# Kernel optimization log

Measured on AMD Instinct MI355X. Metric: run time of the kernel, lower is better.

Reference implementation:

```python
import jax, jax.numpy as jnp
import numpy as np

P = 7          # window size
HEADS = 8
DIM_HEAD = 32
INNER = HEADS * DIM_HEAD  # 256
DIM_IN = 256
DIM_OUT = 256
SCALE = DIM_HEAD ** -0.5


def _rel_index(p):
    i = np.array([[x, y] for x in range(p) for y in range(p)])  # (p*p, 2)
    d = i[None, :, :] - i[:, None, :]                            # (p*p, p*p, 2)
    return jnp.asarray(d + p - 1, dtype=jnp.int32)


def setup_inputs() -> dict:
    key = jax.random.key(0)
    ks = jax.random.split(key, 6)
    x = jax.random.normal(ks[0], (16, DIM_IN, 112, 112), dtype=jnp.float32)
    Wq = jax.random.normal(ks[1], (INNER, DIM_IN), dtype=jnp.float32) * 0.02
    Wkv = jax.random.normal(ks[2], (2 * INNER, DIM_IN), dtype=jnp.float32) * 0.02
    Wo = jax.random.normal(ks[3], (DIM_OUT, INNER), dtype=jnp.float32) * 0.02
    bo = jax.random.normal(ks[4], (DIM_OUT,), dtype=jnp.float32) * 0.02
    pos_embedding = jax.random.normal(ks[5], (2 * P - 1, 2 * P - 1), dtype=jnp.float32) * 0.02
    rel_index = _rel_index(P)
    return {"x": x, "Wq": Wq, "Wkv": Wkv, "Wo": Wo, "bo": bo,
            "pos_embedding": pos_embedding, "rel_index": rel_index}


def _local_attention(x, Wq, Wkv, Wo, bo, pos_embedding, rel_index):
    b, c, h, w = x.shape
    n1, n2 = h // P, w // P
    n = P * P
    # relative position bias (p^2, p^2)
    bias = pos_embedding[rel_index[:, :, 0], rel_index[:, :, 1]]
    # window partition: (b, c, n1, P, n2, P) -> (b*n1*n2, c, P*P)
    xw = x.reshape(b, c, n1, P, n2, P).transpose(0, 2, 4, 1, 3, 5)
    xw = xw.reshape(b * n1 * n2, c, n)
    # 1x1 conv projections as channel GEMMs
    q = jnp.einsum('oc,bcn->bon', Wq, xw)       # (B', INNER, n)
    kv = jnp.einsum('oc,bcn->bon', Wkv, xw)     # (B', 2*INNER, n)
    k, v = kv[:, :INNER], kv[:, INNER:]

    def to_heads(t):  # (B', H*d, n) -> (B', H, n, d)
        Bp = t.shape[0]
        return t.reshape(Bp, HEADS, DIM_HEAD, n).transpose(0, 1, 3, 2)

    q, k, v = to_heads(q), to_heads(k), to_heads(v)
    dots = jnp.einsum('bhid,bhjd->bhij', q, k) * SCALE + bias
    attn = jax.nn.softmax(dots, axis=-1)
    out = jnp.einsum('bhij,bhjd->bhid', attn, v)          # (B', H, n, d)
    out = out.transpose(0, 1, 3, 2).reshape(-1, INNER, n)  # (B', H*d, n)
    out = jnp.einsum('oc,bcn->bon', Wo, out) + bo[None, :, None]
    # window merge back to (b, c_out, h, w)
    out = out.reshape(b, n1, n2, DIM_OUT, P, P).transpose(0, 3, 1, 4, 2, 5)
    out = out.reshape(b, DIM_OUT, h, w)
    return out, attn


def reference(x, Wq, Wkv, Wo, bo, pos_embedding, rel_index):
    return _local_attention(x, Wq, Wkv, Wo, bo, pos_embedding, rel_index)
```

## Files before the change

### kernel.cpp

```cpp
#include <hip/hip_runtime.h>
#include <hip/hip_bf16.h>

typedef __bf16 bf16x8 __attribute__((ext_vector_type(8)));
typedef __bf16 bf16x4 __attribute__((ext_vector_type(4)));
typedef float  f32x4  __attribute__((ext_vector_type(4)));
typedef float  f32x16 __attribute__((ext_vector_type(16)));
typedef float  f32x4a __attribute__((ext_vector_type(4))) __attribute__((aligned(4)));
typedef float  f32x2a __attribute__((ext_vector_type(2))) __attribute__((aligned(4)));

#define NPOS 49
#define NHEADS 8
#define SCALE_F 0.17677669529663687f

#define SLICE_B   16896
#define QK_ROW_B  264
#define VS_OFF    8192
#define VS_ROW_B  136
#define XWT_PITCH 264
#define AOT_PITCH 264
#define BIAS_OFF  67584
#define BO_OFF    77188
#define LDS_BYTES 78212

static __device__ __forceinline__ f32x16 zero16() {
  f32x16 z;
#pragma unroll
  for (int i = 0; i < 16; ++i) z[i] = 0.f;
  return z;
}

__global__ void prep_kernel(const float* __restrict__ Wq, const float* __restrict__ Wkv,
                            const float* __restrict__ Wo, const float* __restrict__ pos,
                            const int* __restrict__ rel, __bf16* __restrict__ wqkv,
                            __bf16* __restrict__ wo, float* __restrict__ bias,
                            __bf16* __restrict__ wqkvP, __bf16* __restrict__ woP) {
  const int idx = blockIdx.x * 256 + threadIdx.x;
  const int row = idx >> 8, col = idx & 255;
  const float wv = (row < 256) ? Wq[idx] : Wkv[idx - 65536];
  wqkv[idx] = (__bf16)wv;
  {
    const int s = row >> 5, l31 = row & 31;
    const int ks = col >> 4, g2 = (col >> 3) & 1, e = col & 7;
    wqkvP[((size_t)((s * 16 + ks) * 64 + g2 * 32 + l31)) * 8 + e] = (__bf16)wv;
  }
  if (idx < 65536) {
    const float w = Wo[idx];
    wo[idx] = (__bf16)w;
    const int t = row >> 4, c16 = row & 15;
    const int kk = col >> 5, g4 = (col >> 3) & 3, e = col & 7;
    woP[((size_t)((t * 8 + kk) * 64 + g4 * 16 + c16)) * 8 + e] = (__bf16)w;
  }
  if (idx < 49 * 49) bias[idx] = pos[rel[idx * 2] * 13 + rel[idx * 2 + 1]];
}

template <int MODE>
__global__ __launch_bounds__(256, 2) void attn_kernel(
    const float* __restrict__ x, const __bf16* __restrict__ wqkvP,
    const __bf16* __restrict__ wo, const float* __restrict__ bias_g,
    const float* __restrict__ bo_g, float* __restrict__ outg,
    float* __restrict__ attng, __bf16* __restrict__ aoT_g) {
  extern __shared__ char smem[];
  __bf16* xwT = (__bf16*)smem;
  __bf16* aoT = (__bf16*)smem;
  float* bias_s = (float*)(smem + BIAS_OFF);
  float* bo_s   = (float*)(smem + BO_OFF);

  const int tid = threadIdx.x;
  const int bid = blockIdx.x;
  const int work = (bid & 7) * 512 + (bid >> 3);
  const int b  = work >> 8;
  const int i1 = (work >> 4) & 15;
  const int i2 = work & 15;
  const int r0 = i1 * 7, c0 = i2 * 7;
  const int wave = tid >> 6, lane = tid & 63;
  const int l31 = lane & 31, g2 = lane >> 5;
  const int c16 = lane & 15, g4 = lane >> 4;
  char* slice = smem + wave * SLICE_B;

  {
    bf16x8 z8;
#pragma unroll
    for (int j = 0; j < 8; ++j) z8[j] = (__bf16)0.f;
    for (int i = tid; i < 480; i += 256) {
      const int row = 49 + (i >> 5);
      const int col = (i & 31) * 8;
      *(bf16x8*)(xwT + row * XWT_PITCH + col) = z8;
    }
    f32x4a b4[7]; f32x2a b2[7]; float b1[7];
    int chv[7], rowv[7];
    const float* xb = x + (size_t)b * 256 * 12544;
#pragma unroll
    for (int k = 0; k < 7; ++k) {
      const int p = k * 256 + tid;
      const int ch = p / 7;
      const int row = p - ch * 7;
      chv[k] = ch; rowv[k] = row;
      const float* xr = xb + (size_t)ch * 12544 + (size_t)(r0 + row) * 112 + c0;
      b4[k] = *(const f32x4a*)xr;
      b2[k] = *(const f32x2a*)(xr + 4);
      b1[k] = xr[6];
    }
#pragma unroll
    for (int k = 0; k < 7; ++k) {
      __bf16* dst = xwT + (rowv[k] * 7) * XWT_PITCH + chv[k];
      dst[0 * XWT_PITCH] = (__bf16)b4[k][0];
      dst[1 * XWT_PITCH] = (__bf16)b4[k][1];
      dst[2 * XWT_PITCH] = (__bf16)b4[k][2];
      dst[3 * XWT_PITCH] = (__bf16)b4[k][3];
      dst[4 * XWT_PITCH] = (__bf16)b2[k][0];
      dst[5 * XWT_PITCH] = (__bf16)b2[k][1];
      dst[6 * XWT_PITCH] = (__bf16)b1[k];
    }
    const float4* bg4 = (const float4*)bias_g;
    for (int i = tid; i < 600; i += 256) ((float4*)bias_s)[i] = bg4[i];
    if (tid == 0) bias_s[2400] = bias_g[2400];
    if constexpr (MODE == 0) bo_s[tid] = bo_g[tid];
  }
  __syncthreads();

  bf16x8 Bf0[16], Bf1[16];
  {
    const __bf16* Bp = xwT + l31 * XWT_PITCH + g2 * 8;
#pragma unroll
    for (int ks = 0; ks < 16; ++ks) {
      Bf0[ks] = *(const bf16x8*)(Bp + ks * 16);
      Bf1[ks] = *(const bf16x8*)(Bp + 32 * XWT_PITCH + ks * 16);
    }
  }
  __syncthreads();

  char* vsb = slice + VS_OFF;
  {
    const __bf16* A0p = wqkvP + (size_t)(16 + 2 * wave) * 8192 + lane * 8;
    const __bf16* A1p = A0p + 8192;
    f32x16 a00 = zero16(), a01 = zero16(), a10 = zero16(), a11 = zero16();
    __builtin_amdgcn_s_setprio(1);
#pragma unroll
    for (int ks = 0; ks < 16; ++ks) {
      bf16x8 A0 = *(const bf16x8*)(A0p + ks * 512);
      bf16x8 A1 = *(const bf16x8*)(A1p + ks * 512);
      a00 = __builtin_amdgcn_mfma_f32_32x32x16_bf16(A0, Bf0[ks], a00, 0, 0, 0);
      a01 = __builtin_amdgcn_mfma_f32_32x32x16_bf16(A0, Bf1[ks], a01, 0, 0, 0);
      a10 = __builtin_amdgcn_mfma_f32_32x32x16_bf16(A1, Bf0[ks], a10, 0, 0, 0);
      a11 = __builtin_amdgcn_mfma_f32_32x32x16_bf16(A1, Bf1[ks], a11, 0, 0, 0);
    }
    __builtin_amdgcn_s_setprio(0);
#pragma unroll
    for (int rg = 0; rg < 16; ++rg) {
      const int dd = (rg & 3) + 8 * (rg >> 2) + 4 * g2;
      *(__bf16*)(vsb + dd * VS_ROW_B + l31 * 2)              = (__bf16)a00[rg];
      *(__bf16*)(vsb + dd * VS_ROW_B + 64 + l31 * 2)         = (__bf16)a01[rg];
      *(__bf16*)(vsb + (32 + dd) * VS_ROW_B + l31 * 2)       = (__bf16)a10[rg];
      *(__bf16*)(vsb + (32 + dd) * VS_ROW_B + 64 + l31 * 2)  = (__bf16)a11[rg];
    }
  }
  bf16x8 vf[2][2][2];
#pragma unroll
  for (int hh = 0; hh < 2; ++hh)
#pragma unroll
    for (int nt = 0; nt < 2; ++nt)
#pragma unroll
      for (int ks = 0; ks < 2; ++ks)
        vf[hh][nt][ks] = *(const bf16x8*)(vsb + (hh * 32 + nt * 16 + c16) * VS_ROW_B + ks * 64 + g4 * 16);
  asm volatile("s_waitcnt lgkmcnt(0)" ::: "memory");
  __builtin_amdgcn_sched_barrier(0x20);

#pragma unroll
  for (int qk = 0; qk < 2; ++qk) {
    const int koff = qk * 64;
    const __bf16* A0p = wqkvP + (size_t)(2 * wave + qk * 8) * 8192 + lane * 8;
    const __bf16* A1p = A0p + 8192;
    f32x16 a00 = zero16(), a01 = zero16(), a10 = zero16(), a11 = zero16();
    __builtin_amdgcn_s_setprio(1);
#pragma unroll
    for (int ks = 0; ks < 16; ++ks) {
      bf16x8 A0 = *(const bf16x8*)(A0p + ks * 512);
      bf16x8 A1 = *(const bf16x8*)(A1p + ks * 512);
      a00 = __builtin_amdgcn_mfma_f32_32x32x16_bf16(A0, Bf0[ks], a00, 0, 0, 0);
      a01 = __builtin_amdgcn_mfma_f32_32x32x16_bf16(A0, Bf1[ks], a01, 0, 0, 0);
      a10 = __builtin_amdgcn_mfma_f32_32x32x16_bf16(A1, Bf0[ks], a10, 0, 0, 0);
      a11 = __builtin_amdgcn_mfma_f32_32x32x16_bf16(A1, Bf1[ks], a11, 0, 0, 0);
    }
    __builtin_amdgcn_s_setprio(0);
#define STORE_QK(ACC, P_, NT)                                                  \
    {                                                                          \
      const int n_ = (NT) * 32 + l31;                                          \
      _Pragma("unroll") for (int rb = 0; rb < 4; ++rb) {                       \
        const int ddb = koff + (P_) * 32 + rb * 8 + g2 * 4;                    \
        bf16x4 v4;                                                             \
        v4[0] = (__bf16)ACC[rb * 4 + 0]; v4[1] = (__bf16)ACC[rb * 4 + 1];      \
        v4[2] = (__bf16)ACC[rb * 4 + 2]; v4[3] = (__bf16)ACC[rb * 4 + 3];      \
        *(bf16x4*)(slice + n_ * QK_ROW_B + ddb * 2) = v4;                      \
      }                                                                        \
    }
    STORE_QK(a00, 0, 0)
    STORE_QK(a01, 0, 1)
    STORE_QK(a10, 1, 0)
    STORE_QK(a11, 1, 1)
  }
  bf16x8 qf[2][4], kf[2][4];
#pragma unroll
  for (int hh = 0; hh < 2; ++hh)
#pragma unroll
    for (int t = 0; t < 4; ++t) {
      qf[hh][t] = *(const bf16x8*)(slice + (t * 16 + c16) * QK_ROW_B + hh * 64 + g4 * 16);
      kf[hh][t] = *(const bf16x8*)(slice + (t * 16 + c16) * QK_ROW_B + 128 + hh * 64 + g4 * 16);
    }
  asm volatile("s_waitcnt lgkmcnt(0)" ::: "memory");
  __builtin_amdgcn_sched_barrier(0x20);

  f32x4 pacc[2][4][2];
  char* Pb0 = slice;
  char* Pb1 = slice + 8192;
  {
    const f32x4 z4 = {0.f, 0.f, 0.f, 0.f};
    f32x4 dacc[2][4][4];
    __builtin_amdgcn_s_setprio(1);
#pragma unroll
    for (int hh = 0; hh < 2; ++hh)
#pragma unroll
      for (int mt = 0; mt < 4; ++mt)
#pragma unroll
        for (int nt = 0; nt < 4; ++nt)
          dacc[hh][mt][nt] = __builtin_amdgcn_mfma_f32_16x16x32_bf16(qf[hh][mt], kf[hh][nt], z4, 0, 0, 0);
    __builtin_amdgcn_s_setprio(0);

    const int h0 = wave * 2;
#pragma unroll
    for (int mt = 0; mt < 4; ++mt) {
#pragma unroll
      for (int r = 0; r < 4; ++r) {
        const int i = mt * 16 + g4 * 4 + r;
        float p0[4], p1[4], s0 = 0.f, s1 = 0.f;
#pragma unroll
        for (int nt = 0; nt < 4; ++nt) {
          const int j = nt * 16 + c16;
          float v0 = dacc[0][mt][nt][r] * SCALE_F;
          float v1 = dacc[1][mt][nt][r] * SCALE_F;
          if (j < NPOS) {
            if (i < NPOS) { const float bb = bias_s[i * 49 + j]; v0 += bb; v1 += bb; }
          } else {
            v0 = -1e30f; v1 = -1e30f;
          }
          p0[nt] = __expf(v0); s0 += p0[nt];
          p1[nt] = __expf(v1); s1 += p1[nt];
        }
        s0 += __shfl_xor(s0, 1); s1 += __shfl_xor(s1, 1);
        s0 += __shfl_xor(s0, 2); s1 += __shfl_xor(s1, 2);
        s0 += __shfl_xor(s0, 4); s1 += __shfl_xor(s1, 4);
        s0 += __shfl_xor(s0, 8); s1 += __shfl_xor(s1, 8);
        const float inv0 = 1.f / s0, inv1 = 1.f / s1;
        if (i < NPOS) {
          float* ap0 = attng + ((size_t)(work * NHEADS + h0) * 49 + i) * 49;
          float* ap1 = ap0 + 49 * 49;
#pragma unroll
          for (int nt = 0; nt < 4; ++nt) {
            const int j = nt * 16 + c16;
            if (j < NPOS) { ap0[j] = p0[nt] * inv0; ap1[j] = p1[nt] * inv1; }
          }
        }
#pragma unroll
        for (int nt = 0; nt < 4; ++nt) {
          const int j = nt * 16 + c16;
          *(__bf16*)(Pb0 + i * 128 + 16 * ((j >> 3) ^ (i & 7)) + 2 * (j & 7)) = (__bf16)(p0[nt] * inv0);
          *(__bf16*)(Pb1 + i * 128 + 16 * ((j >> 3) ^ (i & 7)) + 2 * (j & 7)) = (__bf16)(p1[nt] * inv1);
        }
      }
    }

    __builtin_amdgcn_s_setprio(1);
#pragma unroll
    for (int hh = 0; hh < 2; ++hh) {
      char* Pb = hh ? Pb1 : Pb0;
#pragma unroll
      for (int mt = 0; mt < 4; ++mt) {
        const int i = mt * 16 + c16;
        bf16x8 pa0 = *(const bf16x8*)(Pb + i * 128 + 16 * ((0 + g4) ^ (i & 7)));
        bf16x8 pa1 = *(const bf16x8*)(Pb + i * 128 + 16 * ((4 + g4) ^ (i & 7)));
#pragma unroll
        for (int nt = 0; nt < 2; ++nt) {
          f32x4 acc = {0.f, 0.f, 0.f, 0.f};
          acc = __builtin_amdgcn_mfma_f32_16x16x32_bf16(pa0, vf[hh][nt][0], acc, 0, 0, 0);
          acc = __builtin_amdgcn_mfma_f32_16x16x32_bf16(pa1, vf[hh][nt][1], acc, 0, 0, 0);
          pacc[hh][mt][nt] = acc;
        }
      }
    }
    __builtin_amdgcn_s_setprio(0);
  }

  if constexpr (MODE == 1) {
    __bf16* ag = aoT_g + (size_t)work * 12544;
#pragma unroll
    for (int hh = 0; hh < 2; ++hh) {
      const int h = wave * 2 + hh;
#pragma unroll
      for (int mt = 0; mt < 4; ++mt)
#pragma unroll
        for (int e = 0; e < 4; ++e) {
          const int pos = mt * 16 + g4 * 4 + e;
          if (pos < NPOS) {
            ag[pos * 256 + h * 32 + c16]      = (__bf16)pacc[hh][mt][0][e];
            ag[pos * 256 + h * 32 + 16 + c16] = (__bf16)pacc[hh][mt][1][e];
          }
        }
    }
  } else {
    __syncthreads();
#pragma unroll
    for (int hh = 0; hh < 2; ++hh) {
      const int h = wave * 2 + hh;
#pragma unroll
      for (int mt = 0; mt < 4; ++mt)
#pragma unroll
        for (int nt = 0; nt < 2; ++nt)
#pragma unroll
          for (int e = 0; e < 4; ++e) {
            const int i = mt * 16 + g4 * 4 + e;
            const int cc = h * 32 + nt * 16 + c16;
            aoT[i * AOT_PITCH + cc] = (__bf16)pacc[hh][mt][nt][e];
          }
    }
    __syncthreads();
    {
      bf16x8 Cf0[16], Cf1[16];
      const __bf16* Bp = aoT + l31 * AOT_PITCH + g2 * 8;
#pragma unroll
      for (int ks = 0; ks < 16; ++ks) {
        Cf0[ks] = *(const bf16x8*)(Bp + ks * 16);
        Cf1[ks] = *(const bf16x8*)(Bp + 32 * AOT_PITCH + ks * 16);
      }
      const __bf16* Ap0 = wo + (size_t)(wave * 64 + l31) * 256 + g2 * 8;
      const __bf16* Ap1 = Ap0 + 32 * 256;
      f32x16 a00 = zero16(), a01 = zero16(), a10 = zero16(), a11 = zero16();
      __builtin_amdgcn_s_setprio(1);
#pragma unroll
      for (int ks = 0; ks < 16; ++ks) {
        bf16x8 A0 = *(const bf16x8*)(Ap0 + ks * 16);
        bf16x8 A1 = *(const bf16x8*)(Ap1 + ks * 16);
        a00 = __builtin_amdgcn_mfma_f32_32x32x16_bf16(A0, Cf0[ks], a00, 0, 0, 0);
        a01 = __builtin_amdgcn_mfma_f32_32x32x16_bf16(A0, Cf1[ks], a01, 0, 0, 0);
        a10 = __builtin_amdgcn_mfma_f32_32x32x16_bf16(A1, Cf0[ks], a10, 0, 0, 0);
        a11 = __builtin_amdgcn_mfma_f32_32x32x16_bf16(A1, Cf1[ks], a11, 0, 0, 0);
      }
      __builtin_amdgcn_s_setprio(0);
      float* og = outg + (size_t)b * 256 * 12544;
#define STORE_OUT(ACC, MT, NT)                                                    \
      {                                                                           \
        const int n_ = (NT) * 32 + l31;                                           \
        if (n_ < NPOS) {                                                          \
          const int pr_ = n_ / 7, pc_ = n_ - pr_ * 7;                             \
          float* orow = og + (size_t)(r0 + pr_) * 112 + (c0 + pc_);               \
          _Pragma("unroll") for (int rg = 0; rg < 16; ++rg) {                     \
            const int o2 = wave * 64 + (MT) * 32 + (rg & 3) + 8 * (rg >> 2) + 4 * g2; \
            orow[(size_t)o2 * 12544] = ACC[rg] + bo_s[o2];                        \
          }                                                                       \
        }                                                                         \
      }
      STORE_OUT(a00, 0, 0)
      STORE_OUT(a01, 0, 1)
      STORE_OUT(a10, 1, 0)
      STORE_OUT(a11, 1, 1)
    }
  }
}

__global__ __launch_bounds__(256, 2) void oproj_kernel(
    const __bf16* __restrict__ aoT_g, const __bf16* __restrict__ woP,
    const float* __restrict__ bo_g, float* __restrict__ outg) {
  __shared__ __bf16 aoB[112 * 264];
  __shared__ float bo_s[256];
  const int tid = threadIdx.x;
  const int bid = blockIdx.x;
  const int work = (bid & 7) * 224 + (bid >> 3);
  const int pr = work % 7;
  const int g  = work / 7;
  const int i1 = g & 15, b = g >> 4;
  const int wave = tid >> 6, lane = tid & 63;
  const int c16 = lane & 15, g4 = lane >> 4;

  {
    const int rr = tid >> 5, coff = (tid & 31) * 8;
#pragma unroll
    for (int it = 0; it < 14; ++it) {
      const int gr = it * 8 + rr;
      const int i2 = gr / 7, pc = gr - i2 * 7;
      const size_t src = ((size_t)((b * 256 + i1 * 16 + i2) * 49 + pr * 7 + pc)) * 256 + coff;
      *(bf16x8*)(aoB + gr * 264 + coff) = *(const bf16x8*)(aoT_g + src);
    }
    bo_s[tid] = bo_g[tid];
  }
  __syncthreads();

  const int oc0 = wave * 64;
  const __bf16* Ap = woP + ((size_t)wave * 4 * 8) * 512 + lane * 8;
  f32x4 acc[4][7];
#pragma unroll
  for (int mt = 0; mt < 4; ++mt)
#pragma unroll
    for (int nt = 0; nt < 7; ++nt) acc[mt][nt] = f32x4{0.f, 0.f, 0.f, 0.f};
#pragma unroll
  for (int kk = 0; kk < 8; ++kk) {
    bf16x8 Af[4], Bf[7];
#pragma unroll
    for (int mt = 0; mt < 4; ++mt)
      Af[mt] = *(const bf16x8*)(Ap + (size_t)(mt * 8 + kk) * 512);
#pragma unroll
    for (int nt = 0; nt < 7; ++nt)
      Bf[nt] = *(const bf16x8*)(aoB + (nt * 16 + c16) * 264 + kk * 32 + g4 * 8);
    __builtin_amdgcn_s_setprio(1);
#pragma unroll
    for (int mt = 0; mt < 4; ++mt)
#pragma unroll
      for (int nt = 0; nt < 7; ++nt)
        acc[mt][nt] = __builtin_amdgcn_mfma_f32_16x16x32_bf16(Af[mt], Bf[nt], acc[mt][nt], 0, 0, 0);
    __builtin_amdgcn_s_setprio(0);
  }
  float* orow = outg + (size_t)b * 256 * 12544 + (size_t)(i1 * 7 + pr) * 112;
#pragma unroll
  for (int mt = 0; mt < 4; ++mt)
#pragma unroll
    for (int e = 0; e < 4; ++e) {
      const int oc = oc0 + mt * 16 + g4 * 4 + e;
      const float bb = bo_s[oc];
#pragma unroll
      for (int nt = 0; nt < 7; ++nt)
        orow[(size_t)oc * 12544 + nt * 16 + c16] = acc[mt][nt][e] + bb;
    }
}

extern "C" void kernel_launch(void* const* d_in, const int* in_sizes, int n_in,
                              void* d_out, int out_size, void* d_ws, size_t ws_size,
                              hipStream_t stream) {
  const float* x   = (const float*)d_in[0];
  const float* Wq  = (const float*)d_in[1];
  const float* Wkv = (const float*)d_in[2];
  const float* Wo  = (const float*)d_in[3];
  const float* bo  = (const float*)d_in[4];
  const float* pos = (const float*)d_in[5];
  const int*   rel = (const int*)d_in[6];

  float* outg  = (float*)d_out;
  float* attng = outg + (size_t)16 * 256 * 112 * 112;

  __bf16* wqkv  = (__bf16*)d_ws;
  __bf16* wo    = (__bf16*)((char*)d_ws + 393216);
  float*  bias  = (float*)((char*)d_ws + 393216 + 131072);
  __bf16* wqkvP = (__bf16*)((char*)d_ws + 393216 + 131072 + 9728);
  __bf16* woP   = (__bf16*)((char*)d_ws + 393216 + 131072 + 9728 + 393216);
  size_t base = 393216 + 131072 + 9728 + 393216 + 131072;
  base = (base + 255) & ~(size_t)255;
  const size_t ao_bytes = (size_t)4096 * 12544 * 2;
  __bf16* aoT_g = (__bf16*)((char*)d_ws + base);
  (void)wqkv;

  hipFuncSetAttribute((const void*)attn_kernel<0>,
                      hipFuncAttributeMaxDynamicSharedMemorySize, LDS_BYTES);
  hipFuncSetAttribute((const void*)attn_kernel<1>,
                      hipFuncAttributeMaxDynamicSharedMemorySize, LDS_BYTES);

  prep_kernel<<<dim3(768), dim3(256), 0, stream>>>(Wq, Wkv, Wo, pos, rel, wqkv, wo, bias,
                                                   wqkvP, woP);
  if (ws_size >= base + ao_bytes) {
    attn_kernel<1><<<dim3(4096), dim3(256), LDS_BYTES, stream>>>(
        x, wqkvP, wo, bias, bo, outg, attng, aoT_g);
    oproj_kernel<<<dim3(1792), dim3(256), 0, stream>>>(aoT_g, woP, bo, outg);
  } else {
    attn_kernel<0><<<dim3(4096), dim3(256), LDS_BYTES, stream>>>(
        x, wqkvP, wo, bias, bo, outg, attng, nullptr);
  }
}
```

Before: 426.0 us.

## Shrink per-wave LDS slices and read bias from global to fit three blocks per CU

The per-wave LDS slice is cut by storing only the 49 valid positions and overlapping the V staging and P buffers. The shared-memory copies of the relative bias and output bias are removed, and those values are now read straight from global memory. Total LDS per block falls from about 78KB to about 52KB, and launch bounds are raised to 3 blocks per CU to increase occupancy. The cost is uncached global bias reads inside the softmax loop, extra clamping on row indices, and more register pressure under the tighter launch bound.

```diff
diff --git a/kernel.cpp b/kernel.cpp
--- a/kernel.cpp
+++ b/kernel.cpp
@@ -12,15 +12,13 @@
 #define NHEADS 8
 #define SCALE_F 0.17677669529663687f
 
-#define SLICE_B   16896
+#define SLICE_B   13056
 #define QK_ROW_B  264
-#define VS_OFF    8192
 #define VS_ROW_B  136
+#define P1_OFF    6400
 #define XWT_PITCH 264
 #define AOT_PITCH 264
-#define BIAS_OFF  67584
-#define BO_OFF    77188
-#define LDS_BYTES 78212
+#define LDS_BYTES 52224
 
 static __device__ __forceinline__ f32x16 zero16() {
   f32x16 z;
@@ -54,7 +52,7 @@
 }
 
 template <int MODE>
-__global__ __launch_bounds__(256, 2) void attn_kernel(
+__global__ __launch_bounds__(256, 3) void attn_kernel(
     const float* __restrict__ x, const __bf16* __restrict__ wqkvP,
     const __bf16* __restrict__ wo, const float* __restrict__ bias_g,
     const float* __restrict__ bo_g, float* __restrict__ outg,
@@ -62,8 +60,6 @@
   extern __shared__ char smem[];
   __bf16* xwT = (__bf16*)smem;
   __bf16* aoT = (__bf16*)smem;
-  float* bias_s = (float*)(smem + BIAS_OFF);
-  float* bo_s   = (float*)(smem + BO_OFF);
 
   const int tid = threadIdx.x;
   const int bid = blockIdx.x;
@@ -111,10 +107,6 @@
       dst[5 * XWT_PITCH] = (__bf16)b2[k][1];
       dst[6 * XWT_PITCH] = (__bf16)b1[k];
     }
-    const float4* bg4 = (const float4*)bias_g;
-    for (int i = tid; i < 600; i += 256) ((float4*)bias_s)[i] = bg4[i];
-    if (tid == 0) bias_s[2400] = bias_g[2400];
-    if constexpr (MODE == 0) bo_s[tid] = bo_g[tid];
   }
   __syncthreads();
 
@@ -129,7 +121,7 @@
   }
   __syncthreads();
 
-  char* vsb = slice + VS_OFF;
+  char* vsb = slice;
   {
     const __bf16* A0p = wqkvP + (size_t)(16 + 2 * wave) * 8192 + lane * 8;
     const __bf16* A1p = A0p + 8192;
@@ -185,12 +177,14 @@
 #define STORE_QK(ACC, P_, NT)                                                  \
     {                                                                          \
       const int n_ = (NT) * 32 + l31;                                          \
-      _Pragma("unroll") for (int rb = 0; rb < 4; ++rb) {                       \
-        const int ddb = koff + (P_) * 32 + rb * 8 + g2 * 4;                    \
-        bf16x4 v4;                                                             \
-        v4[0] = (__bf16)ACC[rb * 4 + 0]; v4[1] = (__bf16)ACC[rb * 4 + 1];      \
-        v4[2] = (__bf16)ACC[rb * 4 + 2]; v4[3] = (__bf16)ACC[rb * 4 + 3];      \
-        *(bf16x4*)(slice + n_ * QK_ROW_B + ddb * 2) = v4;                      \
+      if (n_ < NPOS) {                                                         \
+        _Pragma("unroll") for (int rb = 0; rb < 4; ++rb) {                     \
+          const int ddb = koff + (P_) * 32 + rb * 8 + g2 * 4;                  \
+          bf16x4 v4;                                                           \
+          v4[0] = (__bf16)ACC[rb * 4 + 0]; v4[1] = (__bf16)ACC[rb * 4 + 1];    \
+          v4[2] = (__bf16)ACC[rb * 4 + 2]; v4[3] = (__bf16)ACC[rb * 4 + 3];    \
+          *(bf16x4*)(slice + n_ * QK_ROW_B + ddb * 2) = v4;                    \
+        }                                                                      \
       }                                                                        \
     }
     STORE_QK(a00, 0, 0)
@@ -200,18 +194,20 @@
   }
   bf16x8 qf[2][4], kf[2][4];
 #pragma unroll
-  for (int hh = 0; hh < 2; ++hh)
-#pragma unroll
-    for (int t = 0; t < 4; ++t) {
-      qf[hh][t] = *(const bf16x8*)(slice + (t * 16 + c16) * QK_ROW_B + hh * 64 + g4 * 16);
-      kf[hh][t] = *(const bf16x8*)(slice + (t * 16 + c16) * QK_ROW_B + 128 + hh * 64 + g4 * 16);
-    }
+  for (int t = 0; t < 4; ++t) {
+    int rr = t * 16 + c16; rr = rr > 48 ? 48 : rr;
+#pragma unroll
+    for (int hh = 0; hh < 2; ++hh) {
+      qf[hh][t] = *(const bf16x8*)(slice + rr * QK_ROW_B + hh * 64 + g4 * 16);
+      kf[hh][t] = *(const bf16x8*)(slice + rr * QK_ROW_B + 128 + hh * 64 + g4 * 16);
+    }
+  }
   asm volatile("s_waitcnt lgkmcnt(0)" ::: "memory");
   __builtin_amdgcn_sched_barrier(0x20);
 
   f32x4 pacc[2][4][2];
   char* Pb0 = slice;
-  char* Pb1 = slice + 8192;
+  char* Pb1 = slice + P1_OFF;
   {
     const f32x4 z4 = {0.f, 0.f, 0.f, 0.f};
     f32x4 dacc[2][4][4];
@@ -238,7 +234,7 @@
           float v0 = dacc[0][mt][nt][r] * SCALE_F;
           float v1 = dacc[1][mt][nt][r] * SCALE_F;
           if (j < NPOS) {
-            if (i < NPOS) { const float bb = bias_s[i * 49 + j]; v0 += bb; v1 += bb; }
+            if (i < NPOS) { const float bb = bias_g[i * 49 + j]; v0 += bb; v1 += bb; }
           } else {
             v0 = -1e30f; v1 = -1e30f;
           }
@@ -256,15 +252,12 @@
 #pragma unroll
           for (int nt = 0; nt < 4; ++nt) {
             const int j = nt * 16 + c16;
-            if (j < NPOS) { ap0[j] = p0[nt] * inv0; ap1[j] = p1[nt] * inv1; }
+            const float q0 = p0[nt] * inv0, q1 = p1[nt] * inv1;
+            if (j < NPOS) { ap0[j] = q0; ap1[j] = q1; }
+            *(__bf16*)(Pb0 + i * 128 + 16 * ((j >> 3) ^ (i & 7)) + 2 * (j & 7)) = (__bf16)q0;
+            *(__bf16*)(Pb1 + i * 128 + 16 * ((j >> 3) ^ (i & 7)) + 2 * (j & 7)) = (__bf16)q1;
           }
         }
-#pragma unroll
-        for (int nt = 0; nt < 4; ++nt) {
-          const int j = nt * 16 + c16;
-          *(__bf16*)(Pb0 + i * 128 + 16 * ((j >> 3) ^ (i & 7)) + 2 * (j & 7)) = (__bf16)(p0[nt] * inv0);
-          *(__bf16*)(Pb1 + i * 128 + 16 * ((j >> 3) ^ (i & 7)) + 2 * (j & 7)) = (__bf16)(p1[nt] * inv1);
-        }
       }
     }
 
@@ -274,7 +267,7 @@
       char* Pb = hh ? Pb1 : Pb0;
 #pragma unroll
       for (int mt = 0; mt < 4; ++mt) {
-        const int i = mt * 16 + c16;
+        int i = mt * 16 + c16; i = i > 48 ? 48 : i;
         bf16x8 pa0 = *(const bf16x8*)(Pb + i * 128 + 16 * ((0 + g4) ^ (i & 7)));
         bf16x8 pa1 = *(const bf16x8*)(Pb + i * 128 + 16 * ((4 + g4) ^ (i & 7)));
 #pragma unroll
@@ -353,7 +346,7 @@
           float* orow = og + (size_t)(r0 + pr_) * 112 + (c0 + pc_);               \
           _Pragma("unroll") for (int rg = 0; rg < 16; ++rg) {                     \
             const int o2 = wave * 64 + (MT) * 32 + (rg & 3) + 8 * (rg >> 2) + 4 * g2; \
-            orow[(size_t)o2 * 12544] = ACC[rg] + bo_s[o2];                        \
+            orow[(size_t)o2 * 12544] = ACC[rg] + bo_g[o2];                        \
           }                                                                       \
         }                                                                         \
       }
```

Result: slower. 659.1 us (+54.7%).
